# Kernel optimization log

Measured on AMD Instinct MI355X. Metric: run time of the kernel, lower is better.

## Reference

```python
import jax, jax.numpy as jnp
import numpy as np

BS, T = 128, 256
N_AGENTS, STATE_DIM, EMBED_DIM, HYPERNET_EMBED = 32, 512, 64, 256


def setup_inputs() -> dict:
    key = jax.random.key(0)
    ks = jax.random.split(key, 16)
    s = 0.02  # param init scale
    return {
        "agent_qs": jax.random.normal(ks[0], (BS, T, N_AGENTS), jnp.float32),
        "states": jax.random.normal(ks[1], (BS, T, STATE_DIM), jnp.float32),
        "w1_0": jax.random.normal(ks[2], (HYPERNET_EMBED, STATE_DIM), jnp.float32) * s,
        "b1_0": jax.random.normal(ks[3], (HYPERNET_EMBED,), jnp.float32) * s,
        "w1_2": jax.random.normal(ks[4], (EMBED_DIM * N_AGENTS, HYPERNET_EMBED), jnp.float32) * s,
        "b1_2": jax.random.normal(ks[5], (EMBED_DIM * N_AGENTS,), jnp.float32) * s,
        "wf_0": jax.random.normal(ks[6], (HYPERNET_EMBED, STATE_DIM), jnp.float32) * s,
        "bf_0": jax.random.normal(ks[7], (HYPERNET_EMBED,), jnp.float32) * s,
        "wf_2": jax.random.normal(ks[8], (EMBED_DIM, HYPERNET_EMBED), jnp.float32) * s,
        "bf_2": jax.random.normal(ks[9], (EMBED_DIM,), jnp.float32) * s,
        "hb_w": jax.random.normal(ks[10], (EMBED_DIM, STATE_DIM), jnp.float32) * s,
        "hb_b": jax.random.normal(ks[11], (EMBED_DIM,), jnp.float32) * s,
        "v0_w": jax.random.normal(ks[12], (EMBED_DIM, STATE_DIM), jnp.float32) * s,
        "v0_b": jax.random.normal(ks[13], (EMBED_DIM,), jnp.float32) * s,
        "v2_w": jax.random.normal(ks[14], (1, EMBED_DIM), jnp.float32) * s,
        "v2_b": jax.random.normal(ks[15], (1,), jnp.float32) * s,
    }


def reference(agent_qs, states, w1_0, b1_0, w1_2, b1_2, wf_0, bf_0, wf_2, bf_2,
              hb_w, hb_b, v0_w, v0_b, v2_w, v2_b):
    bs = agent_qs.shape[0]
    s = states.reshape(-1, STATE_DIM)          # [B, S]
    q = agent_qs.reshape(-1, 1, N_AGENTS)       # [B, 1, A]
    # hypernet-generated first-layer weights (positive via abs)
    h1 = jax.nn.relu(s @ w1_0.T + b1_0)
    w1 = jnp.abs(h1 @ w1_2.T + b1_2).reshape(-1, N_AGENTS, EMBED_DIM)  # [B, A, E]
    b1 = (s @ hb_w.T + hb_b).reshape(-1, 1, EMBED_DIM)                 # [B, 1, E]
    hidden = jax.nn.elu(jnp.einsum('bia,bae->bie', q, w1) + b1)        # [B, 1, E]
    # hypernet-generated final weights
    hf = jax.nn.relu(s @ wf_0.T + bf_0)
    w_final = jnp.abs(hf @ wf_2.T + bf_2).reshape(-1, EMBED_DIM, 1)    # [B, E, 1]
    v = (jax.nn.relu(s @ v0_w.T + v0_b) @ v2_w.T + v2_b).reshape(-1, 1, 1)
    y = jnp.einsum('bie,beo->bio', hidden, w_final) + v                # [B, 1, 1]
    return y.reshape(bs, -1, 1)
```

## Files before the change

kernel.cpp:

```cpp
#include <hip/hip_runtime.h>


#define SDIM 512
#define HD   256
#define EDIM 64
#define NAG  32

typedef short short8v __attribute__((ext_vector_type(8)));
typedef short short4v __attribute__((ext_vector_type(4)));
typedef float f32x4  __attribute__((ext_vector_type(4)));

__device__ __forceinline__ unsigned short f2bf(float f) {
  unsigned int u = __float_as_uint(f);
  unsigned int r = (u + 0x7FFFu + ((u >> 16) & 1u)) >> 16;
  return (unsigned short)r;
}
__device__ __forceinline__ float bf2f(unsigned short u) {
  return __uint_as_float(((unsigned int)u) << 16);
}
__device__ __forceinline__ short4v cvt4(float4 a) {
  short4v r;
  r[0] = (short)f2bf(a.x); r[1] = (short)f2bf(a.y);
  r[2] = (short)f2bf(a.z); r[3] = (short)f2bf(a.w);
  return r;
}

__global__ void qmix_convert(const float* __restrict__ w1_0, const float* __restrict__ wf_0,
                             const float* __restrict__ hb_w, const float* __restrict__ v0_w,
                             const float* __restrict__ w1_2, const float* __restrict__ wf_2,
                             unsigned short* __restrict__ W0cat, unsigned short* __restrict__ w12b,
                             unsigned short* __restrict__ wf2b) {
  int i = blockIdx.x * 256 + threadIdx.x;
  if (i < 327680) {
    float v;
    if (i < 131072)      v = w1_0[i];
    else if (i < 262144) v = wf_0[i - 131072];
    else if (i < 294912) v = hb_w[i - 262144];
    else                 v = v0_w[i - 294912];
    W0cat[i] = f2bf(v);
  } else if (i < 851968) {
    w12b[i - 327680] = f2bf(w1_2[i - 327680]);
  } else if (i < 868352) {
    wf2b[i - 851968] = f2bf(wf_2[i - 851968]);
  }
}

__global__ __launch_bounds__(512, 1) void qmix_k1(
    const float* __restrict__ states, const unsigned short* __restrict__ W0cat,
    const unsigned short* __restrict__ wf2b,
    const float* __restrict__ b1_0, const float* __restrict__ bf_0,
    const float* __restrict__ hb_b, const float* __restrict__ v0_b,
    const float* __restrict__ v2_w, const float* __restrict__ bf_2,
    unsigned short* __restrict__ h1g, unsigned short* __restrict__ b1h,
    unsigned short* __restrict__ wfinh, float* __restrict__ vbuf)
{
  __shared__ unsigned short sA[64 * 512];
  __shared__ unsigned short bbuf[2][20480];

  const int t    = threadIdx.x;
  const int r0   = blockIdx.x * 64;
  const int wave = t >> 6, lane = t & 63;
  const int lrow = lane & 15, lk = lane >> 4;
  const int rg = wave >> 2;
  const int ch = wave & 3;
  const int colbase = ch * 160;

  const float4* gS4 = (const float4*)(states + (size_t)r0 * SDIM);
  float4 L[16];
#pragma unroll
  for (int it = 0; it < 16; it++) L[it] = gS4[it * 512 + t];

  short8v breg[5];
#pragma unroll
  for (int j = 0; j < 5; j++) {
    int m = j * 512 + t;
    int col = m >> 2, kslot = m & 3;
    breg[j] = *(const short8v*)(W0cat + (size_t)col * SDIM + kslot * 8);
  }

#pragma unroll
  for (int it = 0; it < 16; it++) {
    int idx = it * 512 + t;
    int row = idx >> 7, c4 = idx & 127;
    int byte = (row * 1024 + c4 * 8) ^ ((row & 7) << 4);
    *(short4v*)((char*)sA + byte) = cvt4(L[it]);
  }
#pragma unroll
  for (int j = 0; j < 5; j++) {
    int m = j * 512 + t;
    int col = m >> 2, kslot = m & 3;
    *(short8v*)((char*)bbuf + col * 64 + ((kslot * 16) ^ ((col & 3) << 4))) = breg[j];
  }
  __syncthreads();

  f32x4 acc[2][10];
#pragma unroll
  for (int i = 0; i < 2; i++)
#pragma unroll
    for (int f = 0; f < 10; f++) acc[i][f] = (f32x4){0.f, 0.f, 0.f, 0.f};

#pragma unroll 1
  for (int ks = 0; ks < 16; ks++) {
    if (ks < 15) {
#pragma unroll
      for (int j = 0; j < 5; j++) {
        int m = j * 512 + t;
        int col = m >> 2, kslot = m & 3;
        breg[j] = *(const short8v*)(W0cat + (size_t)col * SDIM + (ks + 1) * 32 + kslot * 8);
      }
    }
    const char* rb = (const char*)bbuf + (ks & 1) * 40960;
    short8v af0, af1;
    {
      int row = rg * 32 + lrow;
      af0 = *(const short8v*)((const char*)sA + ((row * 1024 + ks * 64 + lk * 16) ^ ((row & 7) << 4)));
      row = rg * 32 + 16 + lrow;
      af1 = *(const short8v*)((const char*)sA + ((row * 1024 + ks * 64 + lk * 16) ^ ((row & 7) << 4)));
    }
#pragma unroll
    for (int cf = 0; cf < 10; cf++) {
      int col = colbase + cf * 16 + lrow;
      short8v b = *(const short8v*)(rb + col * 64 + ((lk * 16) ^ ((col & 3) << 4)));
      acc[0][cf] = __builtin_amdgcn_mfma_f32_16x16x32_bf16(af0, b, acc[0][cf], 0, 0, 0);
      acc[1][cf] = __builtin_amdgcn_mfma_f32_16x16x32_bf16(af1, b, acc[1][cf], 0, 0, 0);
    }
    if (ks < 15) {
      char* wb = (char*)bbuf + ((ks + 1) & 1) * 40960;
#pragma unroll
      for (int j = 0; j < 5; j++) {
        int m = j * 512 + t;
        int col = m >> 2, kslot = m & 3;
        *(short8v*)(wb + col * 64 + ((kslot * 16) ^ ((col & 3) << 4))) = breg[j];
      }
    }
    __syncthreads();
  }

  {
    float vs[2][4];
#pragma unroll
    for (int i = 0; i < 2; i++)
#pragma unroll
      for (int rr = 0; rr < 4; rr++) vs[i][rr] = 0.f;

#pragma unroll
    for (int cf = 0; cf < 10; cf++) {
      int cb  = colbase + cf * 16;
      int col = cb + lrow;
      if (cb < 512) {
        float bv = (cb < 256) ? b1_0[col] : bf_0[col - 256];
#pragma unroll
        for (int i = 0; i < 2; i++)
#pragma unroll
          for (int rr = 0; rr < 4; rr++) {
            int row = rg * 32 + i * 16 + lk * 4 + rr;
            float v = fmaxf(acc[i][cf][rr] + bv, 0.f);
            int byte = (row * 1024 + col * 2) ^ ((row & 7) << 4);
            *(unsigned short*)((char*)sA + byte) = f2bf(v);
          }
      } else if (cb < 576) {
        int e = col - 512;
        float bv = hb_b[e];
#pragma unroll
        for (int i = 0; i < 2; i++)
#pragma unroll
          for (int rr = 0; rr < 4; rr++) {
            int row = rg * 32 + i * 16 + lk * 4 + rr;
            b1h[(size_t)(r0 + row) * EDIM + e] = f2bf(acc[i][cf][rr] + bv);
          }
      } else {
        int e = col - 576;
        float bv = v0_b[e], wv = v2_w[e];
#pragma unroll
        for (int i = 0; i < 2; i++)
#pragma unroll
          for (int rr = 0; rr < 4; rr++)
            vs[i][rr] = fmaf(fmaxf(acc[i][cf][rr] + bv, 0.f), wv, vs[i][rr]);
      }
    }
    if (ch == 3) {
#pragma unroll
      for (int i = 0; i < 2; i++)
#pragma unroll
        for (int rr = 0; rr < 4; rr++) {
          float v = vs[i][rr];
#pragma unroll
          for (int m = 1; m < 16; m <<= 1) v += __shfl_xor(v, m, 64);
          if (lrow == 0) vbuf[r0 + rg * 32 + i * 16 + lk * 4 + rr] = v;
        }
    }
  }
  __syncthreads();

  {
    const int wr2 = wave >> 1;
    const int wc2 = wave & 1;
    f32x4 wfa[2];
    wfa[0] = (f32x4){0.f, 0.f, 0.f, 0.f};
    wfa[1] = (f32x4){0.f, 0.f, 0.f, 0.f};
    const int row = wr2 * 16 + lrow;
#pragma unroll
    for (int kf = 0; kf < 8; kf++) {
      int byte = (row * 1024 + 512 + kf * 64 + lk * 16) ^ ((row & 7) << 4);
      short8v af2 = *(const short8v*)((const char*)sA + byte);
#pragma unroll
      for (int j = 0; j < 2; j++) {
        short8v bf2v = *(const short8v*)(wf2b + (size_t)(wc2 * 32 + j * 16 + lrow) * HD + kf * 32 + 8 * lk);
        wfa[j] = __builtin_amdgcn_mfma_f32_16x16x32_bf16(af2, bf2v, wfa[j], 0, 0, 0);
      }
    }
#pragma unroll
    for (int j = 0; j < 2; j++) {
      int e = wc2 * 32 + j * 16 + lrow;
#pragma unroll
      for (int r = 0; r < 4; r++) {
        int row2 = wr2 * 16 + lk * 4 + r;
        wfinh[(size_t)(r0 + row2) * EDIM + e] = f2bf(fabsf(wfa[j][r] + bf_2[e]));
      }
    }
  }

  {
    char* dst = (char*)h1g + (size_t)r0 * 512;
#pragma unroll
    for (int u = 0; u < 4; u++) {
      int idx = u * 512 + t;
      int row = idx >> 5;
      int p   = (idx & 31) * 16;
      short8v v = *(const short8v*)((const char*)sA + row * 1024 + p);
      *(short8v*)(dst + row * 512 + p) = v;
    }
  }
}

__global__ __launch_bounds__(512, 1) void qmix_k2(
    const unsigned short* __restrict__ h1g, const unsigned short* __restrict__ w12b,
    const float* __restrict__ agent_qs, const float* __restrict__ b1_2,
    const unsigned short* __restrict__ b1h, const unsigned short* __restrict__ wfinh,
    const float* __restrict__ vbuf, const float* __restrict__ v2_b,
    float* __restrict__ out)
{
  __shared__ unsigned char h1s[128 * 512];
  __shared__ unsigned short bbuf[2][16384];
  __shared__ float q_t[NAG * 136];
  __shared__ float ypart[2][128];

  const int t    = threadIdx.x;
  const int r0   = blockIdx.x * 128;
  const int wave = t >> 6, lane = t & 63;
  const int lrow = lane & 15, lk = lane >> 4;
  const int wr = wave >> 1;
  const int wc = wave & 1;

  short8v Lh[8];
  {
    const char* src = (const char*)h1g + (size_t)r0 * 512;
#pragma unroll
    for (int it = 0; it < 8; it++)
      Lh[it] = *(const short8v*)(src + (it * 512 + t) * 16);
  }
  const float4* gq = (const float4*)(agent_qs + (size_t)r0 * NAG);
  float4 q0 = gq[t], q1 = gq[512 + t];
  short8v sreg[4];
#pragma unroll
  for (int rd = 0; rd < 4; rd++)
    sreg[rd] = *(const short8v*)(w12b + rd * 4096 + t * 8);

  {
#pragma unroll
    for (int it = 0; it < 8; it++)
      *(short8v*)(h1s + (it * 512 + t) * 16) = Lh[it];
    int row0 = t >> 3, a4 = (t & 7) * 4;
    q_t[(a4 + 0) * 136 + row0] = q0.x;
    q_t[(a4 + 1) * 136 + row0] = q0.y;
    q_t[(a4 + 2) * 136 + row0] = q0.z;
    q_t[(a4 + 3) * 136 + row0] = q0.w;
    int row1 = 64 + row0;
    q_t[(a4 + 0) * 136 + row1] = q1.x;
    q_t[(a4 + 1) * 136 + row1] = q1.y;
    q_t[(a4 + 2) * 136 + row1] = q1.z;
    q_t[(a4 + 3) * 136 + row1] = q1.w;
#pragma unroll
    for (int rd = 0; rd < 4; rd++) {
      int Lo = rd * 8192 + t * 16;
      *(short8v*)((char*)bbuf + (Lo ^ (((Lo >> 9) & 7) << 4))) = sreg[rd];
    }
  }
  __syncthreads();

  short8v afr[2][8];
#pragma unroll
  for (int i = 0; i < 2; i++) {
    int row = wr * 32 + i * 16 + lrow;
#pragma unroll
    for (int kf = 0; kf < 8; kf++)
      afr[i][kf] = *(const short8v*)(h1s + row * 512 + ((kf * 64 + lk * 16) ^ ((row & 7) << 4)));
  }

  f32x4 hac00 = (f32x4){0.f,0.f,0.f,0.f}, hac01 = (f32x4){0.f,0.f,0.f,0.f};
  f32x4 hac10 = (f32x4){0.f,0.f,0.f,0.f}, hac11 = (f32x4){0.f,0.f,0.f,0.f};

#pragma unroll 1
  for (int a = 0; a < NAG; a++) {
    if (a < NAG - 1) {
      const unsigned short* p = w12b + (size_t)(a + 1) * 16384;
#pragma unroll
      for (int rd = 0; rd < 4; rd++)
        sreg[rd] = *(const short8v*)(p + rd * 4096 + t * 8);
    }
    const char* rbase = (const char*)bbuf + (a & 1) * 32768;

    f32x4 T00 = (f32x4){0.f,0.f,0.f,0.f}, T01 = (f32x4){0.f,0.f,0.f,0.f};
    f32x4 T10 = (f32x4){0.f,0.f,0.f,0.f}, T11 = (f32x4){0.f,0.f,0.f,0.f};
    const int e0 = wc * 32 + lrow, e1 = e0 + 16;
#pragma unroll
    for (int kf = 0; kf < 8; kf++) {
      short8v b0  = *(const short8v*)(rbase + ((e0 * 512 + kf * 64 + lk * 16) ^ ((e0 & 7) << 4)));
      short8v b1v = *(const short8v*)(rbase + ((e1 * 512 + kf * 64 + lk * 16) ^ ((e1 & 7) << 4)));
      T00 = __builtin_amdgcn_mfma_f32_16x16x32_bf16(afr[0][kf], b0,  T00, 0, 0, 0);
      T10 = __builtin_amdgcn_mfma_f32_16x16x32_bf16(afr[1][kf], b0,  T10, 0, 0, 0);
      T01 = __builtin_amdgcn_mfma_f32_16x16x32_bf16(afr[0][kf], b1v, T01, 0, 0, 0);
      T11 = __builtin_amdgcn_mfma_f32_16x16x32_bf16(afr[1][kf], b1v, T11, 0, 0, 0);
    }
    float bb0 = b1_2[a * EDIM + e0];
    float bb1 = b1_2[a * EDIM + e1];
    float4 qa = *(const float4*)(&q_t[a * 136 + wr * 32 + lk * 4]);
    float4 qb = *(const float4*)(&q_t[a * 136 + wr * 32 + 16 + lk * 4]);
#pragma unroll
    for (int r = 0; r < 4; r++) {
      float qar = (r == 0) ? qa.x : (r == 1) ? qa.y : (r == 2) ? qa.z : qa.w;
      float qbr = (r == 0) ? qb.x : (r == 1) ? qb.y : (r == 2) ? qb.z : qb.w;
      hac00[r] = fmaf(qar, fabsf(T00[r] + bb0), hac00[r]);
      hac01[r] = fmaf(qar, fabsf(T01[r] + bb1), hac01[r]);
      hac10[r] = fmaf(qbr, fabsf(T10[r] + bb0), hac10[r]);
      hac11[r] = fmaf(qbr, fabsf(T11[r] + bb1), hac11[r]);
    }
    if (a < NAG - 1) {
      char* wb = (char*)bbuf + ((a & 1) ^ 1) * 32768;
#pragma unroll
      for (int rd = 0; rd < 4; rd++) {
        int Lo = rd * 8192 + t * 16;
        *(short8v*)(wb + (Lo ^ (((Lo >> 9) & 7) << 4))) = sreg[rd];
      }
    }
    __syncthreads();
  }

  {
    float ys0[4], ys1[4];
    const int e0 = wc * 32 + lrow, e1 = e0 + 16;
#pragma unroll
    for (int r = 0; r < 4; r++) {
      int row0 = wr * 32 + lk * 4 + r;
      int row1 = row0 + 16;
      size_t g0 = (size_t)(r0 + row0) * EDIM;
      size_t g1 = (size_t)(r0 + row1) * EDIM;
      float p00 = hac00[r] + bf2f(b1h[g0 + e0]);
      float p01 = hac01[r] + bf2f(b1h[g0 + e1]);
      float p10 = hac10[r] + bf2f(b1h[g1 + e0]);
      float p11 = hac11[r] + bf2f(b1h[g1 + e1]);
      float h00 = p00 > 0.f ? p00 : expm1f(p00);
      float h01 = p01 > 0.f ? p01 : expm1f(p01);
      float h10 = p10 > 0.f ? p10 : expm1f(p10);
      float h11 = p11 > 0.f ? p11 : expm1f(p11);
      ys0[r] = h00 * bf2f(wfinh[g0 + e0]) + h01 * bf2f(wfinh[g0 + e1]);
      ys1[r] = h10 * bf2f(wfinh[g1 + e0]) + h11 * bf2f(wfinh[g1 + e1]);
    }
#pragma unroll
    for (int m = 1; m < 16; m <<= 1)
#pragma unroll
      for (int r = 0; r < 4; r++) {
        ys0[r] += __shfl_xor(ys0[r], m, 64);
        ys1[r] += __shfl_xor(ys1[r], m, 64);
      }
    if (lrow == 0) {
#pragma unroll
      for (int r = 0; r < 4; r++) {
        ypart[wc][wr * 32 + lk * 4 + r]      = ys0[r];
        ypart[wc][wr * 32 + 16 + lk * 4 + r] = ys1[r];
      }
    }
  }
  __syncthreads();
  if (t < 128) {
    out[r0 + t] = ypart[0][t] + ypart[1][t] + vbuf[r0 + t] + v2_b[0];
  }
}

extern "C" void kernel_launch(void* const* d_in, const int* in_sizes, int n_in,
                              void* d_out, int out_size, void* d_ws, size_t ws_size,
                              hipStream_t stream) {
  const float* agent_qs = (const float*)d_in[0];
  const float* states   = (const float*)d_in[1];
  const float* w1_0 = (const float*)d_in[2];
  const float* b1_0 = (const float*)d_in[3];
  const float* w1_2 = (const float*)d_in[4];
  const float* b1_2 = (const float*)d_in[5];
  const float* wf_0 = (const float*)d_in[6];
  const float* bf_0 = (const float*)d_in[7];
  const float* wf_2 = (const float*)d_in[8];
  const float* bf_2 = (const float*)d_in[9];
  const float* hb_w = (const float*)d_in[10];
  const float* hb_b = (const float*)d_in[11];
  const float* v0_w = (const float*)d_in[12];
  const float* v0_b = (const float*)d_in[13];
  const float* v2_w = (const float*)d_in[14];
  const float* v2_b = (const float*)d_in[15];

  char* ws = (char*)d_ws;
  unsigned short* W0cat = (unsigned short*)ws;
  unsigned short* w12b  = (unsigned short*)(ws + 655360);
  unsigned short* wf2b  = (unsigned short*)(ws + 1703936);
  unsigned short* h1g   = (unsigned short*)(ws + 1736704);
  unsigned short* b1h   = (unsigned short*)(ws + 18513920);
  unsigned short* wfinh = (unsigned short*)(ws + 22708224);
  float*          vbuf  = (float*)(ws + 26902528);

  qmix_convert<<<3392, 256, 0, stream>>>(w1_0, wf_0, hb_w, v0_w, w1_2, wf_2,
                                         W0cat, w12b, wf2b);
  qmix_k1<<<512, 512, 0, stream>>>(states, W0cat, wf2b, b1_0, bf_0, hb_b, v0_b,
                                   v2_w, bf_2, h1g, b1h, wfinh, vbuf);
  qmix_k2<<<256, 512, 0, stream>>>(h1g, w12b, agent_qs, b1_2, b1h, wfinh, vbuf,
                                   v2_b, (float*)d_out);
}
```

Measured before the change: 106.5 us.

## Enlarge k2 row tile to 192 rows, single-buffer weights, and reswizzle k1 LDS

```diff
diff --git a/kernel.cpp b/kernel.cpp
--- a/kernel.cpp
+++ b/kernel.cpp
@@ -5,6 +5,8 @@
 #define HD   256
 #define EDIM 64
 #define NAG  32
+#define R2   192
+#define NROW 32768
 
 typedef short short8v __attribute__((ext_vector_type(8)));
 typedef short short4v __attribute__((ext_vector_type(4)));
@@ -89,7 +91,8 @@
   for (int j = 0; j < 5; j++) {
     int m = j * 512 + t;
     int col = m >> 2, kslot = m & 3;
-    *(short8v*)((char*)bbuf + col * 64 + ((kslot * 16) ^ ((col & 3) << 4))) = breg[j];
+    int slot = kslot ^ (col & 3) ^ ((col >> 2) & 3);
+    *(short8v*)((char*)bbuf + col * 64 + (slot << 4)) = breg[j];
   }
   __syncthreads();
 
@@ -120,7 +123,8 @@
 #pragma unroll
     for (int cf = 0; cf < 10; cf++) {
       int col = colbase + cf * 16 + lrow;
-      short8v b = *(const short8v*)(rb + col * 64 + ((lk * 16) ^ ((col & 3) << 4)));
+      int slot = lk ^ (col & 3) ^ ((col >> 2) & 3);
+      short8v b = *(const short8v*)(rb + col * 64 + (slot << 4));
       acc[0][cf] = __builtin_amdgcn_mfma_f32_16x16x32_bf16(af0, b, acc[0][cf], 0, 0, 0);
       acc[1][cf] = __builtin_amdgcn_mfma_f32_16x16x32_bf16(af1, b, acc[1][cf], 0, 0, 0);
     }
@@ -130,7 +134,8 @@
       for (int j = 0; j < 5; j++) {
         int m = j * 512 + t;
         int col = m >> 2, kslot = m & 3;
-        *(short8v*)(wb + col * 64 + ((kslot * 16) ^ ((col & 3) << 4))) = breg[j];
+        int slot = kslot ^ (col & 3) ^ ((col >> 2) & 3);
+        *(short8v*)(wb + col * 64 + (slot << 4)) = breg[j];
       }
     }
     __syncthreads();
@@ -240,46 +245,53 @@
     const float* __restrict__ vbuf, const float* __restrict__ v2_b,
     float* __restrict__ out)
 {
-  __shared__ unsigned char h1s[128 * 512];
-  __shared__ unsigned short bbuf[2][16384];
-  __shared__ float q_t[NAG * 136];
-  __shared__ float ypart[2][128];
+  __shared__ unsigned char h1s[R2 * 512];
+  __shared__ unsigned short bbuf[16384];
+  __shared__ float q_t[NAG * 200];
+  __shared__ float ypart[2][R2];
 
   const int t    = threadIdx.x;
-  const int r0   = blockIdx.x * 128;
+  const int r0   = blockIdx.x * R2;
   const int wave = t >> 6, lane = t & 63;
   const int lrow = lane & 15, lk = lane >> 4;
   const int wr = wave >> 1;
   const int wc = wave & 1;
 
-  short8v Lh[8];
-  {
-    const char* src = (const char*)h1g + (size_t)r0 * 512;
-#pragma unroll
-    for (int it = 0; it < 8; it++)
-      Lh[it] = *(const short8v*)(src + (it * 512 + t) * 16);
-  }
-  const float4* gq = (const float4*)(agent_qs + (size_t)r0 * NAG);
-  float4 q0 = gq[t], q1 = gq[512 + t];
+  {
+    short8v Lh[12];
+#pragma unroll
+    for (int it = 0; it < 12; it++) {
+      int c = it * 512 + t;
+      int row = c >> 5;
+      int p   = (c & 31) * 16;
+      long grow = r0 + row; if (grow > NROW - 1) grow = NROW - 1;
+      Lh[it] = *(const short8v*)((const char*)h1g + grow * 512 + p);
+    }
+#pragma unroll
+    for (int it = 0; it < 12; it++) {
+      int c = it * 512 + t;
+      *(short8v*)(h1s + c * 16) = Lh[it];
+    }
+  }
+  {
+    const float4* gq = (const float4*)agent_qs;
+#pragma unroll
+    for (int v = 0; v < 3; v++) {
+      int idx = v * 512 + t;
+      int row = idx >> 3, c4 = (idx & 7) * 4;
+      long grow = r0 + row; if (grow > NROW - 1) grow = NROW - 1;
+      float4 qv = gq[grow * 8 + (idx & 7)];
+      q_t[(c4 + 0) * 200 + row] = qv.x;
+      q_t[(c4 + 1) * 200 + row] = qv.y;
+      q_t[(c4 + 2) * 200 + row] = qv.z;
+      q_t[(c4 + 3) * 200 + row] = qv.w;
+    }
+  }
   short8v sreg[4];
 #pragma unroll
   for (int rd = 0; rd < 4; rd++)
     sreg[rd] = *(const short8v*)(w12b + rd * 4096 + t * 8);
-
-  {
-#pragma unroll
-    for (int it = 0; it < 8; it++)
-      *(short8v*)(h1s + (it * 512 + t) * 16) = Lh[it];
-    int row0 = t >> 3, a4 = (t & 7) * 4;
-    q_t[(a4 + 0) * 136 + row0] = q0.x;
-    q_t[(a4 + 1) * 136 + row0] = q0.y;
-    q_t[(a4 + 2) * 136 + row0] = q0.z;
-    q_t[(a4 + 3) * 136 + row0] = q0.w;
-    int row1 = 64 + row0;
-    q_t[(a4 + 0) * 136 + row1] = q1.x;
-    q_t[(a4 + 1) * 136 + row1] = q1.y;
-    q_t[(a4 + 2) * 136 + row1] = q1.z;
-    q_t[(a4 + 3) * 136 + row1] = q1.w;
+  {
 #pragma unroll
     for (int rd = 0; rd < 4; rd++) {
       int Lo = rd * 8192 + t * 16;
@@ -288,17 +300,14 @@
   }
   __syncthreads();
 
-  short8v afr[2][8];
-#pragma unroll
-  for (int i = 0; i < 2; i++) {
-    int row = wr * 32 + i * 16 + lrow;
-#pragma unroll
-    for (int kf = 0; kf < 8; kf++)
-      afr[i][kf] = *(const short8v*)(h1s + row * 512 + ((kf * 64 + lk * 16) ^ ((row & 7) << 4)));
-  }
-
-  f32x4 hac00 = (f32x4){0.f,0.f,0.f,0.f}, hac01 = (f32x4){0.f,0.f,0.f,0.f};
-  f32x4 hac10 = (f32x4){0.f,0.f,0.f,0.f}, hac11 = (f32x4){0.f,0.f,0.f,0.f};
+  f32x4 hac[3][2];
+#pragma unroll
+  for (int i = 0; i < 3; i++) {
+    hac[i][0] = (f32x4){0.f,0.f,0.f,0.f};
+    hac[i][1] = (f32x4){0.f,0.f,0.f,0.f};
+  }
+
+  const int e0 = wc * 32 + lrow, e1 = e0 + 16;
 
 #pragma unroll 1
   for (int a = 0; a < NAG; a++) {
@@ -308,82 +317,81 @@
       for (int rd = 0; rd < 4; rd++)
         sreg[rd] = *(const short8v*)(p + rd * 4096 + t * 8);
     }
-    const char* rbase = (const char*)bbuf + (a & 1) * 32768;
-
-    f32x4 T00 = (f32x4){0.f,0.f,0.f,0.f}, T01 = (f32x4){0.f,0.f,0.f,0.f};
-    f32x4 T10 = (f32x4){0.f,0.f,0.f,0.f}, T11 = (f32x4){0.f,0.f,0.f,0.f};
-    const int e0 = wc * 32 + lrow, e1 = e0 + 16;
+
+    f32x4 T[3][2];
+#pragma unroll
+    for (int i = 0; i < 3; i++) {
+      T[i][0] = (f32x4){0.f,0.f,0.f,0.f};
+      T[i][1] = (f32x4){0.f,0.f,0.f,0.f};
+    }
 #pragma unroll
     for (int kf = 0; kf < 8; kf++) {
-      short8v b0  = *(const short8v*)(rbase + ((e0 * 512 + kf * 64 + lk * 16) ^ ((e0 & 7) << 4)));
-      short8v b1v = *(const short8v*)(rbase + ((e1 * 512 + kf * 64 + lk * 16) ^ ((e1 & 7) << 4)));
-      T00 = __builtin_amdgcn_mfma_f32_16x16x32_bf16(afr[0][kf], b0,  T00, 0, 0, 0);
-      T10 = __builtin_amdgcn_mfma_f32_16x16x32_bf16(afr[1][kf], b0,  T10, 0, 0, 0);
-      T01 = __builtin_amdgcn_mfma_f32_16x16x32_bf16(afr[0][kf], b1v, T01, 0, 0, 0);
-      T11 = __builtin_amdgcn_mfma_f32_16x16x32_bf16(afr[1][kf], b1v, T11, 0, 0, 0);
+      short8v b0  = *(const short8v*)((const char*)bbuf + ((e0 * 512 + kf * 64 + lk * 16) ^ ((e0 & 7) << 4)));
+      short8v b1v = *(const short8v*)((const char*)bbuf + ((e1 * 512 + kf * 64 + lk * 16) ^ ((e1 & 7) << 4)));
+#pragma unroll
+      for (int i = 0; i < 3; i++) {
+        int row = wr * 48 + i * 16 + lrow;
+        short8v af = *(const short8v*)(h1s + row * 512 + ((kf * 64 + lk * 16) ^ ((row & 7) << 4)));
+        T[i][0] = __builtin_amdgcn_mfma_f32_16x16x32_bf16(af, b0,  T[i][0], 0, 0, 0);
+        T[i][1] = __builtin_amdgcn_mfma_f32_16x16x32_bf16(af, b1v, T[i][1], 0, 0, 0);
+      }
     }
     float bb0 = b1_2[a * EDIM + e0];
     float bb1 = b1_2[a * EDIM + e1];
-    float4 qa = *(const float4*)(&q_t[a * 136 + wr * 32 + lk * 4]);
-    float4 qb = *(const float4*)(&q_t[a * 136 + wr * 32 + 16 + lk * 4]);
-#pragma unroll
-    for (int r = 0; r < 4; r++) {
-      float qar = (r == 0) ? qa.x : (r == 1) ? qa.y : (r == 2) ? qa.z : qa.w;
-      float qbr = (r == 0) ? qb.x : (r == 1) ? qb.y : (r == 2) ? qb.z : qb.w;
-      hac00[r] = fmaf(qar, fabsf(T00[r] + bb0), hac00[r]);
-      hac01[r] = fmaf(qar, fabsf(T01[r] + bb1), hac01[r]);
-      hac10[r] = fmaf(qbr, fabsf(T10[r] + bb0), hac10[r]);
-      hac11[r] = fmaf(qbr, fabsf(T11[r] + bb1), hac11[r]);
-    }
+#pragma unroll
+    for (int i = 0; i < 3; i++) {
+#pragma unroll
+      for (int r = 0; r < 4; r++) {
+        float qv = q_t[a * 200 + wr * 48 + i * 16 + lk * 4 + r];
+        hac[i][0][r] = fmaf(qv, fabsf(T[i][0][r] + bb0), hac[i][0][r]);
+        hac[i][1][r] = fmaf(qv, fabsf(T[i][1][r] + bb1), hac[i][1][r]);
+      }
+    }
+    __syncthreads();
     if (a < NAG - 1) {
-      char* wb = (char*)bbuf + ((a & 1) ^ 1) * 32768;
 #pragma unroll
       for (int rd = 0; rd < 4; rd++) {
         int Lo = rd * 8192 + t * 16;
-        *(short8v*)(wb + (Lo ^ (((Lo >> 9) & 7) << 4))) = sreg[rd];
+        *(short8v*)((char*)bbuf + (Lo ^ (((Lo >> 9) & 7) << 4))) = sreg[rd];
       }
     }
     __syncthreads();
   }
 
   {
-    float ys0[4], ys1[4];
-    const int e0 = wc * 32 + lrow, e1 = e0 + 16;
-#pragma unroll
-    for (int r = 0; r < 4; r++) {
-      int row0 = wr * 32 + lk * 4 + r;
-      int row1 = row0 + 16;
-      size_t g0 = (size_t)(r0 + row0) * EDIM;
-      size_t g1 = (size_t)(r0 + row1) * EDIM;
-      float p00 = hac00[r] + bf2f(b1h[g0 + e0]);
-      float p01 = hac01[r] + bf2f(b1h[g0 + e1]);
-      float p10 = hac10[r] + bf2f(b1h[g1 + e0]);
-      float p11 = hac11[r] + bf2f(b1h[g1 + e1]);
-      float h00 = p00 > 0.f ? p00 : expm1f(p00);
-      float h01 = p01 > 0.f ? p01 : expm1f(p01);
-      float h10 = p10 > 0.f ? p10 : expm1f(p10);
-      float h11 = p11 > 0.f ? p11 : expm1f(p11);
-      ys0[r] = h00 * bf2f(wfinh[g0 + e0]) + h01 * bf2f(wfinh[g0 + e1]);
-      ys1[r] = h10 * bf2f(wfinh[g1 + e0]) + h11 * bf2f(wfinh[g1 + e1]);
-    }
+    float ys[3][4];
+#pragma unroll
+    for (int i = 0; i < 3; i++)
+#pragma unroll
+      for (int r = 0; r < 4; r++) {
+        int row = wr * 48 + i * 16 + lk * 4 + r;
+        long grow = r0 + row; if (grow > NROW - 1) grow = NROW - 1;
+        size_t g = (size_t)grow * EDIM;
+        float p0 = hac[i][0][r] + bf2f(b1h[g + e0]);
+        float p1 = hac[i][1][r] + bf2f(b1h[g + e1]);
+        float h0 = p0 > 0.f ? p0 : expm1f(p0);
+        float h1 = p1 > 0.f ? p1 : expm1f(p1);
+        ys[i][r] = h0 * bf2f(wfinh[g + e0]) + h1 * bf2f(wfinh[g + e1]);
+      }
 #pragma unroll
     for (int m = 1; m < 16; m <<= 1)
 #pragma unroll
-      for (int r = 0; r < 4; r++) {
-        ys0[r] += __shfl_xor(ys0[r], m, 64);
-        ys1[r] += __shfl_xor(ys1[r], m, 64);
-      }
+      for (int i = 0; i < 3; i++)
+#pragma unroll
+        for (int r = 0; r < 4; r++) ys[i][r] += __shfl_xor(ys[i][r], m, 64);
     if (lrow == 0) {
 #pragma unroll
-      for (int r = 0; r < 4; r++) {
-        ypart[wc][wr * 32 + lk * 4 + r]      = ys0[r];
-        ypart[wc][wr * 32 + 16 + lk * 4 + r] = ys1[r];
-      }
+      for (int i = 0; i < 3; i++)
+#pragma unroll
+        for (int r = 0; r < 4; r++)
+          ypart[wc][wr * 48 + i * 16 + lk * 4 + r] = ys[i][r];
     }
   }
   __syncthreads();
-  if (t < 128) {
-    out[r0 + t] = ypart[0][t] + ypart[1][t] + vbuf[r0 + t] + v2_b[0];
+  if (t < R2) {
+    long grow = r0 + t;
+    if (grow < NROW)
+      out[grow] = ypart[0][t] + ypart[1][t] + vbuf[grow] + v2_b[0];
   }
 }
 
@@ -420,6 +428,7 @@
                                          W0cat, w12b, wf2b);
   qmix_k1<<<512, 512, 0, stream>>>(states, W0cat, wf2b, b1_0, bf_0, hb_b, v0_b,
                                    v2_w, bf_2, h1g, b1h, wfinh, vbuf);
-  qmix_k2<<<256, 512, 0, stream>>>(h1g, w12b, agent_qs, b1_2, b1h, wfinh, vbuf,
-                                   v2_b, (float*)d_out);
-}
+  qmix_k2<<<(NROW + R2 - 1) / R2, 512, 0, stream>>>(h1g, w12b, agent_qs, b1_2,
+                                                    b1h, wfinh, vbuf, v2_b,
+                                                    (float*)d_out);
+}
```

Result: slower. 129.6 us (+21.6%).
